# Optimization experiments

Measured on AMD Instinct MI355X. Metric: run time of the kernel, lower is better.

Reference implementation:

```python
import jax, jax.numpy as jnp
import numpy as np

WS, STRIDE, GRID, HW = 3, 2, 4, 9          # window, stride, 4x4 windows, 9x9 grid
HEADS, HEAD_DIM, DIM = 4, 16, 64
INNER = HEADS * HEAD_DIM                    # 64
BATCH = 8192

_RI = (np.arange(GRID) * STRIDE)[:, None] + np.arange(WS)[None, :]   # [4,3] row/col starts+offsets
_coords = np.array([[x, y] for x in range(WS) for y in range(WS)])   # [9,2]
_REL = (_coords[None, :, :] - _coords[:, None, :]) + (WS - 1)        # [9,9,2] in [0,4]


def setup_inputs() -> dict:
    key = jax.random.key(0)
    ks = jax.random.split(key, 6)
    return {
        "x": jax.random.normal(ks[0], (BATCH, HW, HW, DIM), jnp.float32),
        "w_qkv": jax.random.normal(ks[1], (3 * INNER, DIM), jnp.float32) * 0.05,
        "pos_embedding": jax.random.normal(ks[2], (2 * WS - 1, 2 * WS - 1), jnp.float32),
        "w1": jax.random.normal(ks[3], (DIM // 2, INNER), jnp.float32) * 0.05,
        "b1": jnp.zeros((DIM // 2,), jnp.float32),
        "ln_g": jnp.ones((DIM // 2,), jnp.float32),
        "ln_b": jnp.zeros((DIM // 2,), jnp.float32),
        "w2": jax.random.normal(ks[4], (DIM, DIM // 2), jnp.float32) * 0.05,
        "b2": jnp.zeros((DIM,), jnp.float32),
    }


def reference(x, w_qkv, pos_embedding, w1, b1, ln_g, ln_b, w2, b2):
    b = x.shape[0]
    ri = jnp.asarray(_RI)                                  # [4,3]
    rel0 = jnp.asarray(_REL[..., 0]); rel1 = jnp.asarray(_REL[..., 1])

    qkv = jnp.einsum('bhwc,oc->bhwo', x, w_qkv)            # [b,9,9,3*INNER]
    # nn.Unfold(k=3, s=2): overlapping 3x3 windows -> [b,4,4,3,3,3I] -> [b,16,9,3I]
    win = qkv[:, ri[:, None, :, None], ri[None, :, None, :], :]
    win = win.reshape(b, GRID * GRID, WS * WS, 3 * INNER)
    q, k, v = jnp.split(win, 3, axis=-1)

    def to_heads(t):  # [b,n,wh,(h d)] -> [b,h,n,wh,d]
        return t.reshape(b, GRID * GRID, WS * WS, HEADS, HEAD_DIM).transpose(0, 3, 1, 2, 4)
    q, k, v = to_heads(q), to_heads(k), to_heads(v)

    bias = pos_embedding[rel0, rel1]                       # [9,9] relative-position bias
    attn = jnp.einsum('bhwid,bhwjd->bhwij', q, k) * (HEAD_DIM ** -0.5) + bias
    attn = jax.nn.softmax(attn, axis=-1)
    out = jnp.einsum('bhwij,bhwjd->bhwid', attn, v)        # [b,H,16,9,D]

    # rearrange 'b h n wh d -> b (wh h d) n'
    outf = out.transpose(0, 3, 1, 4, 2).reshape(b, WS * WS * INNER, GRID * GRID)
    # nn.Fold interprets channels as (c, kernel_pos) with c = idx // 9; overlaps are summed
    tmp = outf.reshape(b, INNER, WS, WS, GRID, GRID).transpose(0, 4, 5, 2, 3, 1)  # [b,wi,wj,ki,kj,C]
    canvas = jnp.zeros((b, HW, HW, INNER), out.dtype)
    canvas = canvas.at[:, ri[:, None, :, None], ri[None, :, None, :], :].add(tmp)

    h1 = jnp.einsum('bhwc,oc->bhwo', canvas, w1) + b1      # Linear(inner, dim/2)
    mu = jnp.mean(h1, -1, keepdims=True)
    var = jnp.var(h1, -1, keepdims=True)
    h1 = (h1 - mu) * jax.lax.rsqrt(var + 1e-5) * ln_g + ln_b
    h1 = jax.nn.gelu(h1, approximate=False)                # torch nn.GELU default = exact erf
    return jnp.einsum('bhwc,oc->bhwo', h1, w2) + b2        # [b,9,9,DIM]
```

## Files before the change

### kernel.cpp

```cpp
#include <hip/hip_runtime.h>
#include <math.h>

#define BLOCK_ 512
#define BPB_   8
#define NBLK_  (8192/BPB_)

typedef __bf16 bf16x8 __attribute__((ext_vector_type(8)));
typedef float  f32x4  __attribute__((ext_vector_type(4)));
typedef unsigned short us8 __attribute__((ext_vector_type(8)));

#define XS_  72
#define WQS_ 72
#define QKS_ 136
#define VS_  68
#define CS_  68
#define W1S_ 72
#define W2S_ 40
#define HGS_ 40

struct alignas(16) Smem {
    unsigned short Xb[2][96*XS_];
    unsigned short Wq[192*WQS_];
    unsigned short QK[96*QKS_];
    float          Vf[96*VS_];
    float          Cv[96*CS_];
    unsigned short W1[32*W1S_];
    unsigned short W2[64*W2S_];
    float Bias[81];
    float B1v[32], LnG[32], LnB[32], B2v[64];
};

__device__ __forceinline__ unsigned short f2bf(float f) {
    union { float f; unsigned u; } v; v.f = f;
    unsigned r = v.u + 0x7FFFu + ((v.u >> 16) & 1u);
    return (unsigned short)(r >> 16);
}
__device__ __forceinline__ float bf2f(unsigned short b) {
    union { float f; unsigned u; } v; v.u = ((unsigned)b) << 16;
    return v.f;
}
__device__ __forceinline__ us8 pack8(float4 a, float4 b) {
    us8 r;
    r[0]=f2bf(a.x); r[1]=f2bf(a.y); r[2]=f2bf(a.z); r[3]=f2bf(a.w);
    r[4]=f2bf(b.x); r[5]=f2bf(b.y); r[6]=f2bf(b.z); r[7]=f2bf(b.w);
    return r;
}
__device__ __forceinline__ f32x4 mfma16(us8 a, us8 b, f32x4 c) {
    return __builtin_amdgcn_mfma_f32_16x16x32_bf16(
        __builtin_bit_cast(bf16x8, a), __builtin_bit_cast(bf16x8, b), c, 0, 0, 0);
}

__global__ __launch_bounds__(BLOCK_, 2)
void wattn_mfma(const float* __restrict__ x, const float* __restrict__ w_qkv,
                const float* __restrict__ pe, const float* __restrict__ w1,
                const float* __restrict__ b1, const float* __restrict__ lng,
                const float* __restrict__ lnb, const float* __restrict__ w2,
                const float* __restrict__ b2, float* __restrict__ out)
{
    __shared__ Smem sm;
    const int t = threadIdx.x;
    const int wv = t >> 6, lane = t & 63;
    const int lrow = lane & 15;
    const int lk   = (lane >> 4) * 8;
    const int g4   = (lane >> 4) * 4;

    for (int task = t; task < 192*8; task += BLOCK_) {
        int p = task >> 3, c8 = task & 7;
        const float4* src = (const float4*)(w_qkv + p*64 + c8*8);
        *(us8*)&sm.Wq[p*WQS_ + c8*8] = pack8(src[0], src[1]);
    }
    for (int task = t; task < 32*8; task += BLOCK_) {
        int p = task >> 3, c8 = task & 7;
        const float4* src = (const float4*)(w1 + p*64 + c8*8);
        *(us8*)&sm.W1[p*W1S_ + c8*8] = pack8(src[0], src[1]);
    }
    for (int task = t; task < 64*4; task += BLOCK_) {
        int p = task >> 2, c8 = task & 3;
        const float4* src = (const float4*)(w2 + p*32 + c8*8);
        *(us8*)&sm.W2[p*W2S_ + c8*8] = pack8(src[0], src[1]);
    }
    if (t < 32) { sm.B1v[t]=b1[t]; sm.LnG[t]=lng[t]; sm.LnB[t]=lnb[t]; }
    if (t >= 64 && t < 128) sm.B2v[t-64] = b2[t-64];
    if (t >= 128 && t < 209) {
        int ij = t-128; int i = ij/9, j = ij%9;
        sm.Bias[ij] = pe[((j/3)-(i/3)+2)*5 + ((j%3)-(i%3)+2)];
    }
    for (int idx = t; idx < 96*CS_; idx += BLOCK_) sm.Cv[idx] = 0.f;
    for (int idx = t; idx < 2*15*XS_; idx += BLOCK_) {
        int bsel = idx / (15*XS_); int rem = idx % (15*XS_);
        sm.Xb[bsel][(81 + rem/XS_)*XS_ + rem%XS_] = 0;
    }
    {
        const float* xb = x + (size_t)blockIdx.x * BPB_ * (81*64);
        for (int task = t; task < 648; task += BLOCK_) {
            int p = task >> 3, c8 = task & 7;
            const float4* src = (const float4*)(xb + p*64 + c8*8);
            *(us8*)&sm.Xb[0][p*XS_ + c8*8] = pack8(src[0], src[1]);
        }
    }
    __syncthreads();

    for (int bi = 0; bi < BPB_; ++bi) {
        const int cur = bi & 1;
        const size_t b = (size_t)blockIdx.x * BPB_ + bi;

        float4 pA0, pA1, pB0, pB1;
        const bool hasPF = (bi + 1 < BPB_);
        const bool hasPF2 = hasPF && (t < 136);
        if (hasPF) {
            const float4* xn = (const float4*)(x + (b+1)*(81*64));
            pA0 = xn[t*2]; pA1 = xn[t*2+1];
            if (hasPF2) { pB0 = xn[(512+t)*2]; pB1 = xn[(512+t)*2+1]; }
        }

        {
            const int mg = wv >> 2, ng = wv & 3;
            us8 af[3][2];
            #pragma unroll
            for (int mi = 0; mi < 3; ++mi)
                #pragma unroll
                for (int k = 0; k < 2; ++k)
                    af[mi][k] = *(const us8*)&sm.Xb[cur][(mg*48 + mi*16 + lrow)*XS_ + k*32 + lk];
            #pragma unroll
            for (int ni = 0; ni < 3; ++ni) {
                const int n = ng*3 + ni;
                f32x4 acc[3] = {{0,0,0,0},{0,0,0,0},{0,0,0,0}};
                #pragma unroll
                for (int k = 0; k < 2; ++k) {
                    us8 bf = *(const us8*)&sm.Wq[(n*16 + lrow)*WQS_ + k*32 + lk];
                    #pragma unroll
                    for (int mi = 0; mi < 3; ++mi)
                        acc[mi] = mfma16(af[mi][k], bf, acc[mi]);
                }
                #pragma unroll
                for (int mi = 0; mi < 3; ++mi) {
                    const int row0 = mg*48 + mi*16 + g4;
                    if (n < 8) {
                        #pragma unroll
                        for (int r = 0; r < 4; ++r)
                            sm.QK[(row0+r)*QKS_ + n*16 + lrow] = f2bf(acc[mi][r]);
                    } else {
                        #pragma unroll
                        for (int r = 0; r < 4; ++r)
                            sm.Vf[(row0+r)*VS_ + (n-8)*16 + lrow] = acc[mi][r];
                    }
                }
            }
        }
        __syncthreads();

        for (int task = t; task < 576; task += BLOCK_) {
            int w = task/36, rem = task%36, h = rem/9, i = rem%9;
            int r0 = (w>>2)*2, c0 = (w&3)*2;
            int posq = (r0 + i/3)*9 + (c0 + i%3);
            float q[16];
            {
                us8 u0 = *(const us8*)&sm.QK[posq*QKS_ + h*16];
                us8 u1 = *(const us8*)&sm.QK[posq*QKS_ + h*16 + 8];
                #pragma unroll
                for (int jj=0;jj<8;++jj){ q[jj]=bf2f(u0[jj]); q[8+jj]=bf2f(u1[jj]); }
            }
            float l[9]; float mx = -1e30f;
            #pragma unroll
            for (int j = 0; j < 9; ++j) {
                int posk = (r0 + j/3)*9 + (c0 + j%3);
                us8 u0 = *(const us8*)&sm.QK[posk*QKS_ + 64 + h*16];
                us8 u1 = *(const us8*)&sm.QK[posk*QKS_ + 64 + h*16 + 8];
                float s = 0.f;
                #pragma unroll
                for (int jj=0;jj<8;++jj) s += q[jj]*bf2f(u0[jj]) + q[8+jj]*bf2f(u1[jj]);
                l[j] = s*0.25f + sm.Bias[i*9+j];
                mx = fmaxf(mx, l[j]);
            }
            float ssum = 0.f;
            #pragma unroll
            for (int j=0;j<9;++j){ l[j]=__expf(l[j]-mx); ssum+=l[j]; }
            float inv = 1.f/ssum;
            float o[16];
            #pragma unroll
            for (int d=0; d<16; ++d) o[d]=0.f;
            #pragma unroll
            for (int j = 0; j < 9; ++j) {
                float a = l[j]*inv;
                int posv = (r0 + j/3)*9 + (c0 + j%3);
                const float* vr = &sm.Vf[posv*VS_ + h*16];
                #pragma unroll
                for (int d4=0; d4<4; ++d4) {
                    float4 v = *(const float4*)&vr[d4*4];
                    o[d4*4+0]+=a*v.x; o[d4*4+1]+=a*v.y; o[d4*4+2]+=a*v.z; o[d4*4+3]+=a*v.w;
                }
            }
            int base576 = i*64 + h*16;
            #pragma unroll
            for (int d=0; d<16; ++d) {
                int idx = base576 + d;
                int c = idx/9, r = idx - 9*c;
                int row = (r0 + r/3)*9 + (c0 + r%3);
                atomicAdd(&sm.Cv[row*CS_ + c], o[d]);
            }
        }
        if (hasPF) {
            int p = t >> 3, c8 = t & 7;
            *(us8*)&sm.Xb[cur^1][p*XS_ + c8*8] = pack8(pA0, pA1);
            if (hasPF2) {
                int task = 512 + t; p = task >> 3; c8 = task & 7;
                *(us8*)&sm.Xb[cur^1][p*XS_ + c8*8] = pack8(pB0, pB1);
            }
        }
        __syncthreads();

        if (wv < 6) {
            const int m = wv;
            us8 aF[2];
            #pragma unroll
            for (int k = 0; k < 2; ++k) {
                const float* cp = &sm.Cv[(m*16+lrow)*CS_ + k*32 + lk];
                float4 c0v = *(const float4*)cp;
                float4 c1v = *(const float4*)(cp+4);
                aF[k] = pack8(c0v, c1v);
            }
            f32x4 a0 = {0,0,0,0}, a1 = {0,0,0,0};
            #pragma unroll
            for (int k = 0; k < 2; ++k) {
                us8 b0 = *(const us8*)&sm.W1[lrow*W1S_ + k*32 + lk];
                us8 b1f = *(const us8*)&sm.W1[(16+lrow)*W1S_ + k*32 + lk];
                a0 = mfma16(aF[k], b0, a0);
                a1 = mfma16(aF[k], b1f, a1);
            }
            float bb0 = sm.B1v[lrow],    bb1 = sm.B1v[16+lrow];
            float gg0 = sm.LnG[lrow],    gg1 = sm.LnG[16+lrow];
            float ee0 = sm.LnB[lrow],    ee1 = sm.LnB[16+lrow];
            float v0[4], v1[4], srow[4], qrow[4];
            #pragma unroll
            for (int r=0;r<4;++r) {
                v0[r] = a0[r] + bb0; v1[r] = a1[r] + bb1;
                srow[r] = v0[r] + v1[r];
                qrow[r] = v0[r]*v0[r] + v1[r]*v1[r];
            }
            #pragma unroll
            for (int mask = 1; mask <= 8; mask <<= 1) {
                #pragma unroll
                for (int r=0;r<4;++r) {
                    srow[r] += __shfl_xor(srow[r], mask);
                    qrow[r] += __shfl_xor(qrow[r], mask);
                }
            }
            unsigned short* H1g = sm.QK;
            #pragma unroll
            for (int r=0;r<4;++r) {
                float mean = srow[r]*(1.f/32.f);
                float var  = qrow[r]*(1.f/32.f) - mean*mean;
                float rs   = rsqrtf(var + 1e-5f);
                int row = m*16 + g4 + r;
                float xn0 = (v0[r]-mean)*rs*gg0 + ee0;
                float xn1 = (v1[r]-mean)*rs*gg1 + ee1;
                float ge0 = 0.5f*xn0*(1.f + erff(xn0*0.70710678118654752f));
                float ge1 = 0.5f*xn1*(1.f + erff(xn1*0.70710678118654752f));
                H1g[row*HGS_ + lrow]      = f2bf(ge0);
                H1g[row*HGS_ + 16 + lrow] = f2bf(ge1);
            }
        }
        __syncthreads();

        {
            const unsigned short* H1g = sm.QK;
            #pragma unroll
            for (int ti = 0; ti < 3; ++ti) {
                int ft = wv*3 + ti;
                int m = ft >> 2, n = ft & 3;
                us8 aH = *(const us8*)&H1g[(m*16+lrow)*HGS_ + lk];
                us8 bW = *(const us8*)&sm.W2[(n*16+lrow)*W2S_ + lk];
                f32x4 acc = {0,0,0,0};
                acc = mfma16(aH, bW, acc);
                float bb = sm.B2v[n*16+lrow];
                int row0 = m*16 + g4;
                #pragma unroll
                for (int r=0;r<4;++r) {
                    int row = row0 + r;
                    if (row < 81)
                        out[(b*81 + (size_t)row)*64 + n*16 + lrow] = acc[r] + bb;
                }
            }
        }
        for (int idx = t; idx < 96*CS_; idx += BLOCK_) sm.Cv[idx] = 0.f;
        __syncthreads();
    }
}

extern "C" void kernel_launch(void* const* d_in, const int* in_sizes, int n_in,
                              void* d_out, int out_size, void* d_ws, size_t ws_size,
                              hipStream_t stream) {
    const float* x     = (const float*)d_in[0];
    const float* w_qkv = (const float*)d_in[1];
    const float* pe    = (const float*)d_in[2];
    const float* w1    = (const float*)d_in[3];
    const float* b1    = (const float*)d_in[4];
    const float* lng   = (const float*)d_in[5];
    const float* lnb   = (const float*)d_in[6];
    const float* w2    = (const float*)d_in[7];
    const float* b2    = (const float*)d_in[8];
    float* outp = (float*)d_out;

    wattn_mfma<<<dim3(NBLK_), dim3(BLOCK_), 0, stream>>>(
        x, w_qkv, pe, w1, b1, lng, lnb, w2, b2, outp);
}
```

Measured before the change: 640.8 us.

## Shrink shared memory to raise occupancy: register-resident Wqkv, bf16 V, single X buffer

Removes the shared-memory copy of the QKV weight matrix and instead keeps each wave's B fragments in registers. It also drops the X double buffer, since the prefetch is already staged through registers, stores V as bf16 instead of fp32, and trims the padded rows to 81. Launch bounds go from 2 to 4 blocks per SM so more blocks can be resident to hide latency. The trade-offs are extra register pressure under the tighter launch bound, which could cause spills, added bounds checks on padded rows, and slightly lower precision for V.

```diff
diff --git a/kernel.cpp b/kernel.cpp
--- a/kernel.cpp
+++ b/kernel.cpp
@@ -10,20 +10,18 @@
 typedef unsigned short us8 __attribute__((ext_vector_type(8)));
 
 #define XS_  72
-#define WQS_ 72
 #define QKS_ 136
-#define VS_  68
+#define VS_  72
 #define CS_  68
 #define W1S_ 72
 #define W2S_ 40
 #define HGS_ 40
 
 struct alignas(16) Smem {
-    unsigned short Xb[2][96*XS_];
-    unsigned short Wq[192*WQS_];
-    unsigned short QK[96*QKS_];
-    float          Vf[96*VS_];
-    float          Cv[96*CS_];
+    unsigned short Xb[96*XS_];
+    unsigned short QK[81*QKS_];
+    unsigned short Vf[81*VS_];
+    float          Cv[81*CS_];
     unsigned short W1[32*W1S_];
     unsigned short W2[64*W2S_];
     float Bias[81];
@@ -50,7 +48,7 @@
         __builtin_bit_cast(bf16x8, a), __builtin_bit_cast(bf16x8, b), c, 0, 0, 0);
 }
 
-__global__ __launch_bounds__(BLOCK_, 2)
+__global__ __launch_bounds__(BLOCK_, 4)
 void wattn_mfma(const float* __restrict__ x, const float* __restrict__ w_qkv,
                 const float* __restrict__ pe, const float* __restrict__ w1,
                 const float* __restrict__ b1, const float* __restrict__ lng,
@@ -64,11 +62,16 @@
     const int lk   = (lane >> 4) * 8;
     const int g4   = (lane >> 4) * 4;
 
-    for (int task = t; task < 192*8; task += BLOCK_) {
-        int p = task >> 3, c8 = task & 7;
-        const float4* src = (const float4*)(w_qkv + p*64 + c8*8);
-        *(us8*)&sm.Wq[p*WQS_ + c8*8] = pack8(src[0], src[1]);
-    }
+    const int ng = wv & 3, mg = wv >> 2;
+    us8 bq[3][2];
+    #pragma unroll
+    for (int ni = 0; ni < 3; ++ni)
+        #pragma unroll
+        for (int k = 0; k < 2; ++k) {
+            const float4* src = (const float4*)(w_qkv + ((ng*3+ni)*16 + lrow)*64 + k*32 + lk);
+            bq[ni][k] = pack8(src[0], src[1]);
+        }
+
     for (int task = t; task < 32*8; task += BLOCK_) {
         int p = task >> 3, c8 = task & 7;
         const float4* src = (const float4*)(w1 + p*64 + c8*8);
@@ -85,23 +88,20 @@
         int ij = t-128; int i = ij/9, j = ij%9;
         sm.Bias[ij] = pe[((j/3)-(i/3)+2)*5 + ((j%3)-(i%3)+2)];
     }
-    for (int idx = t; idx < 96*CS_; idx += BLOCK_) sm.Cv[idx] = 0.f;
-    for (int idx = t; idx < 2*15*XS_; idx += BLOCK_) {
-        int bsel = idx / (15*XS_); int rem = idx % (15*XS_);
-        sm.Xb[bsel][(81 + rem/XS_)*XS_ + rem%XS_] = 0;
-    }
+    for (int idx = t; idx < 81*CS_; idx += BLOCK_) sm.Cv[idx] = 0.f;
+    for (int idx = t; idx < 15*XS_; idx += BLOCK_)
+        sm.Xb[(81 + idx/XS_)*XS_ + idx%XS_] = 0;
     {
         const float* xb = x + (size_t)blockIdx.x * BPB_ * (81*64);
         for (int task = t; task < 648; task += BLOCK_) {
             int p = task >> 3, c8 = task & 7;
             const float4* src = (const float4*)(xb + p*64 + c8*8);
-            *(us8*)&sm.Xb[0][p*XS_ + c8*8] = pack8(src[0], src[1]);
+            *(us8*)&sm.Xb[p*XS_ + c8*8] = pack8(src[0], src[1]);
         }
     }
     __syncthreads();
 
     for (int bi = 0; bi < BPB_; ++bi) {
-        const int cur = bi & 1;
         const size_t b = (size_t)blockIdx.x * BPB_ + bi;
 
         float4 pA0, pA1, pB0, pB1;
@@ -114,35 +114,40 @@
         }
 
         {
-            const int mg = wv >> 2, ng = wv & 3;
             us8 af[3][2];
             #pragma unroll
             for (int mi = 0; mi < 3; ++mi)
                 #pragma unroll
                 for (int k = 0; k < 2; ++k)
-                    af[mi][k] = *(const us8*)&sm.Xb[cur][(mg*48 + mi*16 + lrow)*XS_ + k*32 + lk];
+                    af[mi][k] = *(const us8*)&sm.Xb[(mg*48 + mi*16 + lrow)*XS_ + k*32 + lk];
             #pragma unroll
             for (int ni = 0; ni < 3; ++ni) {
                 const int n = ng*3 + ni;
-                f32x4 acc[3] = {{0,0,0,0},{0,0,0,0},{0,0,0,0}};
-                #pragma unroll
-                for (int k = 0; k < 2; ++k) {
-                    us8 bf = *(const us8*)&sm.Wq[(n*16 + lrow)*WQS_ + k*32 + lk];
+                f32x4 acc[3];
+                #pragma unroll
+                for (int mi = 0; mi < 3; ++mi) {
+                    acc[mi][0]=0.f; acc[mi][1]=0.f; acc[mi][2]=0.f; acc[mi][3]=0.f;
+                }
+                #pragma unroll
+                for (int k = 0; k < 2; ++k)
                     #pragma unroll
                     for (int mi = 0; mi < 3; ++mi)
-                        acc[mi] = mfma16(af[mi][k], bf, acc[mi]);
-                }
+                        acc[mi] = mfma16(af[mi][k], bq[ni][k], acc[mi]);
                 #pragma unroll
                 for (int mi = 0; mi < 3; ++mi) {
                     const int row0 = mg*48 + mi*16 + g4;
                     if (n < 8) {
                         #pragma unroll
-                        for (int r = 0; r < 4; ++r)
-                            sm.QK[(row0+r)*QKS_ + n*16 + lrow] = f2bf(acc[mi][r]);
+                        for (int r = 0; r < 4; ++r) {
+                            int row = row0 + r;
+                            if (row < 81) sm.QK[row*QKS_ + n*16 + lrow] = f2bf(acc[mi][r]);
+                        }
                     } else {
                         #pragma unroll
-                        for (int r = 0; r < 4; ++r)
-                            sm.Vf[(row0+r)*VS_ + (n-8)*16 + lrow] = acc[mi][r];
+                        for (int r = 0; r < 4; ++r) {
+                            int row = row0 + r;
+                            if (row < 81) sm.Vf[row*VS_ + (n-8)*16 + lrow] = f2bf(acc[mi][r]);
+                        }
                     }
                 }
             }
@@ -183,11 +188,12 @@
             for (int j = 0; j < 9; ++j) {
                 float a = l[j]*inv;
                 int posv = (r0 + j/3)*9 + (c0 + j%3);
-                const float* vr = &sm.Vf[posv*VS_ + h*16];
-                #pragma unroll
-                for (int d4=0; d4<4; ++d4) {
-                    float4 v = *(const float4*)&vr[d4*4];
-                    o[d4*4+0]+=a*v.x; o[d4*4+1]+=a*v.y; o[d4*4+2]+=a*v.z; o[d4*4+3]+=a*v.w;
+                us8 v0 = *(const us8*)&sm.Vf[posv*VS_ + h*16];
+                us8 v1 = *(const us8*)&sm.Vf[posv*VS_ + h*16 + 8];
+                #pragma unroll
+                for (int jj=0;jj<8;++jj) {
+                    o[jj]   += a * bf2f(v0[jj]);
+                    o[8+jj] += a * bf2f(v1[jj]);
                 }
             }
             int base576 = i*64 + h*16;
@@ -201,35 +207,40 @@
         }
         if (hasPF) {
             int p = t >> 3, c8 = t & 7;
-            *(us8*)&sm.Xb[cur^1][p*XS_ + c8*8] = pack8(pA0, pA1);
+            *(us8*)&sm.Xb[p*XS_ + c8*8] = pack8(pA0, pA1);
             if (hasPF2) {
                 int task = 512 + t; p = task >> 3; c8 = task & 7;
-                *(us8*)&sm.Xb[cur^1][p*XS_ + c8*8] = pack8(pB0, pB1);
+                *(us8*)&sm.Xb[p*XS_ + c8*8] = pack8(pB0, pB1);
             }
         }
         __syncthreads();
 
         if (wv < 6) {
             const int m = wv;
+            const int arow = m*16 + lrow;
             us8 aF[2];
             #pragma unroll
             for (int k = 0; k < 2; ++k) {
-                const float* cp = &sm.Cv[(m*16+lrow)*CS_ + k*32 + lk];
-                float4 c0v = *(const float4*)cp;
-                float4 c1v = *(const float4*)(cp+4);
-                aF[k] = pack8(c0v, c1v);
-            }
-            f32x4 a0 = {0,0,0,0}, a1 = {0,0,0,0};
+                #pragma unroll
+                for (int e=0;e<8;++e) aF[k][e] = 0;
+                if (arow < 81) {
+                    const float* cp = &sm.Cv[arow*CS_ + k*32 + lk];
+                    aF[k] = pack8(*(const float4*)cp, *(const float4*)(cp+4));
+                }
+            }
+            f32x4 a0, a1;
+            a0[0]=0.f; a0[1]=0.f; a0[2]=0.f; a0[3]=0.f;
+            a1[0]=0.f; a1[1]=0.f; a1[2]=0.f; a1[3]=0.f;
             #pragma unroll
             for (int k = 0; k < 2; ++k) {
-                us8 b0 = *(const us8*)&sm.W1[lrow*W1S_ + k*32 + lk];
+                us8 b0  = *(const us8*)&sm.W1[lrow*W1S_ + k*32 + lk];
                 us8 b1f = *(const us8*)&sm.W1[(16+lrow)*W1S_ + k*32 + lk];
                 a0 = mfma16(aF[k], b0, a0);
                 a1 = mfma16(aF[k], b1f, a1);
             }
-            float bb0 = sm.B1v[lrow],    bb1 = sm.B1v[16+lrow];
-            float gg0 = sm.LnG[lrow],    gg1 = sm.LnG[16+lrow];
-            float ee0 = sm.LnB[lrow],    ee1 = sm.LnB[16+lrow];
+            float bb0 = sm.B1v[lrow], bb1 = sm.B1v[16+lrow];
+            float gg0 = sm.LnG[lrow], gg1 = sm.LnG[16+lrow];
+            float ee0 = sm.LnB[lrow], ee1 = sm.LnB[16+lrow];
             float v0[4], v1[4], srow[4], qrow[4];
             #pragma unroll
             for (int r=0;r<4;++r) {
@@ -238,26 +249,27 @@
                 qrow[r] = v0[r]*v0[r] + v1[r]*v1[r];
             }
             #pragma unroll
-            for (int mask = 1; mask <= 8; mask <<= 1) {
+            for (int mask = 1; mask <= 8; mask <<= 1)
                 #pragma unroll
                 for (int r=0;r<4;++r) {
                     srow[r] += __shfl_xor(srow[r], mask);
                     qrow[r] += __shfl_xor(qrow[r], mask);
                 }
-            }
             unsigned short* H1g = sm.QK;
             #pragma unroll
             for (int r=0;r<4;++r) {
-                float mean = srow[r]*(1.f/32.f);
-                float var  = qrow[r]*(1.f/32.f) - mean*mean;
-                float rs   = rsqrtf(var + 1e-5f);
                 int row = m*16 + g4 + r;
-                float xn0 = (v0[r]-mean)*rs*gg0 + ee0;
-                float xn1 = (v1[r]-mean)*rs*gg1 + ee1;
-                float ge0 = 0.5f*xn0*(1.f + erff(xn0*0.70710678118654752f));
-                float ge1 = 0.5f*xn1*(1.f + erff(xn1*0.70710678118654752f));
-                H1g[row*HGS_ + lrow]      = f2bf(ge0);
-                H1g[row*HGS_ + 16 + lrow] = f2bf(ge1);
+                if (row < 81) {
+                    float mean = srow[r]*(1.f/32.f);
+                    float var  = qrow[r]*(1.f/32.f) - mean*mean;
+                    float rs   = rsqrtf(var + 1e-5f);
+                    float xn0 = (v0[r]-mean)*rs*gg0 + ee0;
+                    float xn1 = (v1[r]-mean)*rs*gg1 + ee1;
+                    float ge0 = 0.5f*xn0*(1.f + erff(xn0*0.70710678118654752f));
+                    float ge1 = 0.5f*xn1*(1.f + erff(xn1*0.70710678118654752f));
+                    H1g[row*HGS_ + lrow]      = f2bf(ge0);
+                    H1g[row*HGS_ + 16 + lrow] = f2bf(ge1);
+                }
             }
         }
         __syncthreads();
@@ -268,10 +280,15 @@
             for (int ti = 0; ti < 3; ++ti) {
                 int ft = wv*3 + ti;
                 int m = ft >> 2, n = ft & 3;
-                us8 aH = *(const us8*)&H1g[(m*16+lrow)*HGS_ + lk];
+                int arow = m*16 + lrow;
+                us8 aH;
+                #pragma unroll
+                for (int e=0;e<8;++e) aH[e] = 0;
+                if (arow < 81) aH = *(const us8*)&H1g[arow*HGS_ + lk];
                 us8 bW = *(const us8*)&sm.W2[(n*16+lrow)*W2S_ + lk];
-                f32x4 acc = {0,0,0,0};
-                acc = mfma16(aH, bW, acc);
+                f32x4 zz;
+                zz[0]=0.f; zz[1]=0.f; zz[2]=0.f; zz[3]=0.f;
+                f32x4 acc = mfma16(aH, bW, zz);
                 float bb = sm.B2v[n*16+lrow];
                 int row0 = m*16 + g4;
                 #pragma unroll
@@ -282,7 +299,7 @@
                 }
             }
         }
-        for (int idx = t; idx < 96*CS_; idx += BLOCK_) sm.Cv[idx] = 0.f;
+        for (int idx = t; idx < 81*CS_; idx += BLOCK_) sm.Cv[idx] = 0.f;
         __syncthreads();
     }
 }
```

New measurement: 765.8 us. 19.5% more time.
